# Performance work log

Measured on AMD Instinct MI355X. Metric: run time of the kernel, lower is better.

Reference implementation:

```python
import jax, jax.numpy as jnp
import numpy as np

K = 8  # repeat(1,1,1,9) in the source forces k+1 == 9
LRELU_SLOPE = 0.01  # nn.LeakyReLU default negative slope


def knn_idx(x, k):
    """x: [B, C, N] -> indices of k nearest points [B, N, k] (largest neg sq dist)."""
    xx = jnp.sum(x * x, axis=1)                       # [B, N]
    inner = jnp.einsum('bcn,bcm->bnm', x, x)          # [B, N, N]
    neg_sq_dist = 2.0 * inner - xx[:, :, None] - xx[:, None, :]
    return jax.lax.top_k(neg_sq_dist, k)[1]           # [B, N, k]


def gather_neighbors(feat, idx):
    """feat: [B, C, N], idx: [B, N, k] -> [B, C, N, k] (grouping_operation)."""
    return jax.vmap(lambda f, i: f[:, i])(feat, idx)


def setup_inputs() -> dict:
    key = jax.random.key(0)
    k1, k2, k3 = jax.random.split(key, 3)
    B, C, N = 8, 128, 4096
    points = jax.random.normal(k1, (B, C, N), dtype=jnp.float32)
    # xavier_uniform-ish init for W [C, 1]
    limit = 1.414 * np.sqrt(6.0 / (C + 1))
    W = jax.random.uniform(k2, (C, 1), dtype=jnp.float32, minval=-limit, maxval=limit)
    conv2_w = jax.random.normal(k3, (C, C), dtype=jnp.float32) * 0.05
    return {"points": points, "W": W, "conv2_w": conv2_w}


def reference(points, W, conv2_w):
    # points: [B, C, N]
    shortcut = points
    # knn on raw (detached) features -> integer indices, no grad path
    idx = knn_idx(jax.lax.stop_gradient(points), K)            # [B, N, K]
    features = jax.nn.leaky_relu(points, LRELU_SLOPE)          # [B, C, N]
    grouped_points = gather_neighbors(features, idx)           # [B, C, N, K]
    center_points = features[:, :, :, None]                    # [B, C, N, 1]
    feats = jnp.concatenate([grouped_points, center_points], axis=3)  # [B, C, N, K+1]
    feats = jnp.transpose(feats, (0, 2, 3, 1))                 # [B, N, K+1, C]
    att = jnp.einsum('bnkc,co->bnko', feats, W)                # [B, N, K+1, 1]
    att = jax.nn.softmax(att, axis=2)                          # softmax over K+1 neighbors
    # repeat(1,1,1,9) then matmul: out[b,n,i,c] = att[b,n,i] * sum_j feats[b,n,j,c]
    # followed by mean over i -> mean_i(att) * sum_j(feats)
    s = jnp.sum(feats, axis=2)                                 # [B, N, C]
    out = jnp.mean(att, axis=2) * s                            # [B, N, C]
    out = jnp.transpose(out, (0, 2, 1)) + shortcut             # [B, C, N]
    # 1x1 conv residual branch on grouped neighbor features
    grouped_points_nn = jnp.einsum('oc,bcnk->bonk', conv2_w, grouped_points)  # [B, C, N, K]
    return (out, grouped_points_nn)
```

## Files before the change

### kernel.cpp

```cpp
#include <hip/hip_runtime.h>
#include <cstdint>
#include <cstddef>

#define BB_ 8
#define CC_ 128
#define NN_ 4096
#define KK_ 8

#define XX_OFF  0
#define IDX_OFF 32768
#define G_OFF   294912

__device__ __forceinline__ float lrelu(float v) { return v >= 0.f ? v : 0.01f * v; }

template <int S>
__device__ __forceinline__ void insert_tieup(float (&v)[S], int (&ix)[S], float d, int m) {
  if (d < v[S - 1]) return;
  bool bs[S];
#pragma unroll
  for (int s = 0; s < S; ++s) bs[s] = (v[s] > d);
#pragma unroll
  for (int s = S - 1; s >= 1; --s) {
    v[s]  = bs[s] ? v[s]  : (bs[s - 1] ? d : v[s - 1]);
    ix[s] = bs[s] ? ix[s] : (bs[s - 1] ? m : ix[s - 1]);
  }
  if (!bs[0]) { v[0] = d; ix[0] = m; }
}

template <int S>
__device__ __forceinline__ void insert_ti_desc(float (&v)[S], int (&ix)[S], float d, int m) {
  bool stay = (v[S - 1] > d) || (v[S - 1] == d && ix[S - 1] > m);
  if (stay) return;
  bool bs[S];
#pragma unroll
  for (int s = 0; s < S; ++s) bs[s] = (v[s] > d) || (v[s] == d && ix[s] > m);
#pragma unroll
  for (int s = S - 1; s >= 1; --s) {
    v[s]  = bs[s] ? v[s]  : (bs[s - 1] ? d : v[s - 1]);
    ix[s] = bs[s] ? ix[s] : (bs[s - 1] ? m : ix[s - 1]);
  }
  if (!bs[0]) { v[0] = d; ix[0] = m; }
}

__global__ void k_xx(const float* __restrict__ x, float* __restrict__ out1f) {
  int t = blockIdx.x * 256 + threadIdx.x;
  int b = t >> 12, n = t & (NN_ - 1);
  const float* p = x + ((size_t)b * CC_) * NN_ + n;
  float acc = 0.f;
  {
#pragma clang fp contract(off)
#pragma unroll
    for (int c = 0; c < CC_; ++c) {
      float v = p[(size_t)c * NN_];
      float v2 = v * v;
      acc = acc + v2;
    }
  }
  out1f[XX_OFF + t] = acc;
}

__global__ __launch_bounds__(256, 2) void k_knn(const float* __restrict__ x,
                                                float* __restrict__ out1f) {
  __shared__ __align__(16) union S {
    struct {
      float As[64][132];
      float Bs[64][132];
      float xxm[64];
    } a;
    struct { float v[64 * 129]; int i[64 * 129]; } mg;
  } s;

  const float* xxz = out1f + XX_OFF;
  int* idxz = (int*)(out1f + IDX_OFF);

  const int blk = blockIdx.x;
  const int b = blk >> 6;
  const int n0 = (blk & 63) << 6;
  const float* xb = x + ((size_t)b * CC_) * NN_;
  const int t = threadIdx.x;
  const int tr = t & 15, tc = t >> 4;

  {
    int r = t & 63, c0 = t >> 6;
    for (int c = c0; c < CC_; c += 4) s.a.As[r][c] = xb[(size_t)c * NN_ + n0 + r];
  }

  float xr[4];
#pragma unroll
  for (int i = 0; i < 4; ++i) xr[i] = xxz[(b << 12) + n0 + tr + 16 * i];

  float lv[4][8]; int li[4][8];
#pragma unroll
  for (int i = 0; i < 4; ++i)
#pragma unroll
    for (int q = 0; q < 8; ++q) { lv[i][q] = -INFINITY; li[i][q] = 0x7FFFFFFF; }

  for (int m0 = 0; m0 < NN_; m0 += 64) {
    __syncthreads();
    {
      int ml = t & 63, c1 = t >> 6;
      for (int c = c1; c < CC_; c += 4) s.a.Bs[ml][c] = xb[(size_t)c * NN_ + m0 + ml];
      if (t < 64) s.a.xxm[t] = xxz[(b << 12) + m0 + t];
    }
    __syncthreads();

    float acc[4][4] = {};
#pragma unroll 2
    for (int cq = 0; cq < CC_; cq += 4) {
      float4 av[4], bv[4];
#pragma unroll
      for (int i = 0; i < 4; ++i)
        av[i] = *reinterpret_cast<const float4*>(&s.a.As[tr + 16 * i][cq]);
#pragma unroll
      for (int j = 0; j < 4; ++j)
        bv[j] = *reinterpret_cast<const float4*>(&s.a.Bs[tc * 4 + j][cq]);
#pragma unroll
      for (int i = 0; i < 4; ++i)
#pragma unroll
        for (int j = 0; j < 4; ++j) {
          acc[i][j] = fmaf(av[i].x, bv[j].x, acc[i][j]);
          acc[i][j] = fmaf(av[i].y, bv[j].y, acc[i][j]);
          acc[i][j] = fmaf(av[i].z, bv[j].z, acc[i][j]);
          acc[i][j] = fmaf(av[i].w, bv[j].w, acc[i][j]);
        }
    }

#pragma unroll
    for (int j = 0; j < 4; ++j) {
      float xm = s.a.xxm[tc * 4 + j];
      int m = m0 + tc * 4 + j;
#pragma unroll
      for (int i = 0; i < 4; ++i) {
        float d = (2.0f * acc[i][j] - xr[i]) - xm;
        insert_tieup<8>(lv[i], li[i], d, m);
      }
    }
  }

  __syncthreads();
#pragma unroll
  for (int i = 0; i < 4; ++i) {
    int base = (tr + 16 * i) * 129 + (tc << 3);
#pragma unroll
    for (int q = 0; q < 8; ++q) {
      s.mg.v[base + q] = lv[i][q];
      s.mg.i[base + q] = li[i][q];
    }
  }
  __syncthreads();
  if (t < 64) {
    float bv[8]; int bi[8];
#pragma unroll
    for (int q = 0; q < 8; ++q) { bv[q] = -INFINITY; bi[q] = 0x7FFFFFFF; }
    const float* cv = s.mg.v + t * 129;
    const int*   ci = s.mg.i + t * 129;
    for (int q = 0; q < 128; ++q) {
      insert_ti_desc<8>(bv, bi, cv[q], ci[q]);
    }
    int* op = idxz + (b << 15) + ((n0 + t) << 3);
#pragma unroll
    for (int q = 0; q < KK_; ++q) op[q] = bi[q];
  }
}

__global__ __launch_bounds__(256) void k_gemm(const float* __restrict__ x,
                                              const float* __restrict__ w2,
                                              float* __restrict__ out1f) {
  __shared__ __align__(16) float Ws[64][68];
  __shared__ __align__(16) float Fs[64][68];
  int bb = blockIdx.x >> 7;
  int r = blockIdx.x & 127;
  int o0 = (r >> 6) << 6;
  int m0 = (r & 63) << 6;
  const float* xb = x + ((size_t)bb * CC_) * NN_;
  float* gb = out1f + G_OFF + ((size_t)bb * CC_) * NN_;
  int t = threadIdx.x;
  int tm = t & 15, to = t >> 4;

  float acc[4][4] = {};
  for (int cc = 0; cc < CC_; cc += 64) {
    __syncthreads();
    {
      int cl = t & 63, q0 = t >> 6;
      for (int oo = q0; oo < 64; oo += 4) Ws[oo][cl] = w2[(o0 + oo) * CC_ + cc + cl];
      for (int c2 = q0; c2 < 64; c2 += 4) Fs[cl][c2] = lrelu(xb[(size_t)(cc + c2) * NN_ + m0 + cl]);
    }
    __syncthreads();
#pragma unroll 8
    for (int cq = 0; cq < 64; cq += 4) {
      float4 aw[4], bf[4];
#pragma unroll
      for (int i = 0; i < 4; ++i) aw[i] = *reinterpret_cast<const float4*>(&Ws[to + 16 * i][cq]);
#pragma unroll
      for (int j = 0; j < 4; ++j) bf[j] = *reinterpret_cast<const float4*>(&Fs[tm + 16 * j][cq]);
#pragma unroll
      for (int i = 0; i < 4; ++i)
#pragma unroll
        for (int j = 0; j < 4; ++j) {
          acc[i][j] = fmaf(aw[i].x, bf[j].x, acc[i][j]);
          acc[i][j] = fmaf(aw[i].y, bf[j].y, acc[i][j]);
          acc[i][j] = fmaf(aw[i].z, bf[j].z, acc[i][j]);
          acc[i][j] = fmaf(aw[i].w, bf[j].w, acc[i][j]);
        }
    }
  }
#pragma unroll
  for (int i = 0; i < 4; ++i)
#pragma unroll
    for (int j = 0; j < 4; ++j)
      gb[((size_t)(o0 + to + 16 * i)) * NN_ + m0 + tm + 16 * j] = acc[i][j];
}

__global__ void k_out0(const float* __restrict__ x, const float* __restrict__ out1f,
                       float* __restrict__ out) {
  __shared__ int idxL[512];
  int b = blockIdx.x >> 6, nt = blockIdx.x & 63;
  int n0 = nt << 6;
  int t = threadIdx.x;
  const int* ib = (const int*)(out1f + IDX_OFF) + (b << 15) + (n0 << 3);
  idxL[t] = ib[t];
  idxL[t + 256] = ib[t + 256];
  __syncthreads();
  int nl = t & 63, c0 = t >> 6;
  for (int c = c0; c < CC_; c += 4) {
    const float* row = x + ((size_t)b * CC_ + c) * NN_;
    float self = row[n0 + nl];
    float s = 0.f;
#pragma unroll
    for (int k = 0; k < KK_; ++k) s += lrelu(row[idxL[(nl << 3) + k]]);
    s += lrelu(self);
    out[((size_t)b * CC_ + c) * NN_ + n0 + nl] = fmaf(s, 1.0f / 9.0f, self);
  }
}

__global__ void k_gatherA(float* __restrict__ out1f) {
  int bc = 137 + blockIdx.x;
  int b = bc >> 7;
  const int* idxz = (const int*)(out1f + IDX_OFF) + (b << 15);
  const float* gs = out1f + G_OFF + (size_t)bc * (size_t)NN_;
  float* op = out1f + (size_t)bc * 32768;
  for (int e = threadIdx.x; e < 32768; e += 256) {
    op[e] = gs[idxz[e]];
  }
}

__global__ __launch_bounds__(256) void k_gatherB(const float* __restrict__ x,
                                                 const float* __restrict__ w2,
                                                 float* __restrict__ out1f) {
  __shared__ int idxL[512];
  __shared__ float xcols[8][128];
  int T = blockIdx.x;
  int t = threadIdx.x;
  const int* idxz = (const int*)(out1f + IDX_OFF);
  idxL[t]       = idxz[0 * 32768 + ((T * 32) << 3) + t];
  idxL[t + 256] = idxz[1 * 32768 + ((T * 32) << 3) + t];
  __syncthreads();

  for (int it = 0; it < 64; ++it) {
    int colbase = it * 8;
    {
      int cg = t >> 5, lane = t & 31;
      int col = colbase + cg;
      int bsel = col >> 8;
      int m = idxL[col];
      const float* xb = x + ((size_t)bsel * CC_) * NN_;
#pragma unroll
      for (int q = 0; q < 4; ++q) {
        int c = lane + 32 * q;
        xcols[cg][c] = lrelu(xb[(size_t)c * NN_ + m]);
      }
    }
    __syncthreads();
    {
      int cg = t >> 5, c0 = t & 31;
      int col = colbase + cg;
      int bsel = col >> 8;
      int rk = col & 255;
      int n = T * 32 + (rk >> 3);
      int k = rk & 7;
      int hmax = (bsel == 0) ? 4 : 1;
      for (int h = 0; h < hmax; ++h) {
        int c = c0 + 32 * h;
        const float* wr = w2 + c * CC_;
        float acc = 0.f;
#pragma unroll 8
        for (int cc = 0; cc < CC_; ++cc) acc = fmaf(wr[cc], xcols[cg][cc], acc);
        if (bsel == 0 || c <= 8) {
          out1f[(size_t)(bsel * CC_ + c) * 32768 + (n << 3) + k] = acc;
        }
      }
    }
    __syncthreads();
  }
}

extern "C" void kernel_launch(void* const* d_in, const int* in_sizes, int n_in,
                              void* d_out, int out_size, void* d_ws, size_t ws_size,
                              hipStream_t stream) {
  const float* x  = (const float*)d_in[0];
  const float* w2 = (const float*)d_in[2];

  float* out0  = (float*)d_out;
  float* out1f = out0 + (size_t)BB_ * CC_ * NN_;
  (void)d_ws; (void)ws_size;

  k_xx     <<<(BB_ * NN_) / 256,  256, 0, stream>>>(x, out1f);
  k_knn    <<<BB_ * (NN_ / 64),   256, 0, stream>>>(x, out1f);
  k_gemm   <<<BB_ * 128,          256, 0, stream>>>(x, w2, out1f);
  k_out0   <<<BB_ * 64,           256, 0, stream>>>(x, out1f, out0);
  k_gatherA<<<1024 - 137,         256, 0, stream>>>(out1f);
  k_gatherB<<<128,                256, 0, stream>>>(x, w2, out1f);
}
```

Before: 2.182 ms.

## Swizzle KNN shared-memory tiles and double-buffer LDS reads in the dot loop

Replaces the padded [64][132] shared tiles with unpadded 128-wide rows whose float4 groups are XOR-swizzled by row, so the strided LDS float4 reads avoid bank conflicts. The inner product loop is rewritten to register double-buffer the next float4 group while computing FMAs on the current one. This is meant to cut LDS bank-conflict stalls and hide LDS latency in the distance GEMM. In exchange it needs more live registers under launch_bounds(256,2), and the index arithmetic gets more complex.

```diff
diff --git a/kernel.cpp b/kernel.cpp
--- a/kernel.cpp
+++ b/kernel.cpp
@@ -59,12 +59,39 @@
   out1f[XX_OFF + t] = acc;
 }
 
+__device__ __forceinline__ int swzw(int r, int c) {
+  return (r << 7) + ((((c >> 2) ^ (r & 15)) << 2) | (c & 3));
+}
+
+__device__ __forceinline__ void fma16(float (&acc)[4][4], const float4 (&a)[4],
+                                      const float4 (&b)[4]) {
+#pragma unroll
+  for (int i = 0; i < 4; ++i)
+#pragma unroll
+    for (int j = 0; j < 4; ++j) {
+      acc[i][j] = fmaf(a[i].x, b[j].x, acc[i][j]);
+      acc[i][j] = fmaf(a[i].y, b[j].y, acc[i][j]);
+      acc[i][j] = fmaf(a[i].z, b[j].z, acc[i][j]);
+      acc[i][j] = fmaf(a[i].w, b[j].w, acc[i][j]);
+    }
+}
+
+__device__ __forceinline__ void load8(float4 (&a)[4], float4 (&b)[4],
+                                      const float4* AsV, const float4* BsV,
+                                      const int (&baseA)[4], const int (&baseB)[4],
+                                      const int (&keyB)[4], int tr, int g) {
+#pragma unroll
+  for (int i = 0; i < 4; ++i) a[i] = AsV[baseA[i] + (g ^ tr)];
+#pragma unroll
+  for (int j = 0; j < 4; ++j) b[j] = BsV[baseB[j] + (g ^ keyB[j])];
+}
+
 __global__ __launch_bounds__(256, 2) void k_knn(const float* __restrict__ x,
                                                 float* __restrict__ out1f) {
   __shared__ __align__(16) union S {
     struct {
-      float As[64][132];
-      float Bs[64][132];
+      float As[64 * 128];
+      float Bs[64 * 128];
       float xxm[64];
     } a;
     struct { float v[64 * 129]; int i[64 * 129]; } mg;
@@ -82,7 +109,7 @@
 
   {
     int r = t & 63, c0 = t >> 6;
-    for (int c = c0; c < CC_; c += 4) s.a.As[r][c] = xb[(size_t)c * NN_ + n0 + r];
+    for (int c = c0; c < CC_; c += 4) s.a.As[swzw(r, c)] = xb[(size_t)c * NN_ + n0 + r];
   }
 
   float xr[4];
@@ -94,36 +121,40 @@
   for (int i = 0; i < 4; ++i)
 #pragma unroll
     for (int q = 0; q < 8; ++q) { lv[i][q] = -INFINITY; li[i][q] = 0x7FFFFFFF; }
+
+  const float4* AsV = reinterpret_cast<const float4*>(s.a.As);
+  const float4* BsV = reinterpret_cast<const float4*>(s.a.Bs);
+  int baseA[4], baseB[4], keyB[4];
+#pragma unroll
+  for (int i = 0; i < 4; ++i) baseA[i] = (tr + 16 * i) * 32;
+#pragma unroll
+  for (int j = 0; j < 4; ++j) {
+    int rB = tc * 4 + j;
+    baseB[j] = rB * 32;
+    keyB[j] = rB & 15;
+  }
 
   for (int m0 = 0; m0 < NN_; m0 += 64) {
     __syncthreads();
     {
       int ml = t & 63, c1 = t >> 6;
-      for (int c = c1; c < CC_; c += 4) s.a.Bs[ml][c] = xb[(size_t)c * NN_ + m0 + ml];
+      for (int c = c1; c < CC_; c += 4) s.a.Bs[swzw(ml, c)] = xb[(size_t)c * NN_ + m0 + ml];
       if (t < 64) s.a.xxm[t] = xxz[(b << 12) + m0 + t];
     }
     __syncthreads();
 
     float acc[4][4] = {};
-#pragma unroll 2
-    for (int cq = 0; cq < CC_; cq += 4) {
-      float4 av[4], bv[4];
-#pragma unroll
-      for (int i = 0; i < 4; ++i)
-        av[i] = *reinterpret_cast<const float4*>(&s.a.As[tr + 16 * i][cq]);
-#pragma unroll
-      for (int j = 0; j < 4; ++j)
-        bv[j] = *reinterpret_cast<const float4*>(&s.a.Bs[tc * 4 + j][cq]);
-#pragma unroll
-      for (int i = 0; i < 4; ++i)
-#pragma unroll
-        for (int j = 0; j < 4; ++j) {
-          acc[i][j] = fmaf(av[i].x, bv[j].x, acc[i][j]);
-          acc[i][j] = fmaf(av[i].y, bv[j].y, acc[i][j]);
-          acc[i][j] = fmaf(av[i].z, bv[j].z, acc[i][j]);
-          acc[i][j] = fmaf(av[i].w, bv[j].w, acc[i][j]);
-        }
-    }
+    float4 a0[4], b0[4], a1[4], b1[4];
+    load8(a0, b0, AsV, BsV, baseA, baseB, keyB, tr, 0);
+    for (int g = 0; g < 30; g += 2) {
+      load8(a1, b1, AsV, BsV, baseA, baseB, keyB, tr, g + 1);
+      fma16(acc, a0, b0);
+      load8(a0, b0, AsV, BsV, baseA, baseB, keyB, tr, g + 2);
+      fma16(acc, a1, b1);
+    }
+    load8(a1, b1, AsV, BsV, baseA, baseB, keyB, tr, 31);
+    fma16(acc, a0, b0);
+    fma16(acc, a1, b1);
 
 #pragma unroll
     for (int j = 0; j < 4; ++j) {
```

After: 2.288 ms. +4.9%, slower.

## Shrink kNN shared memory, split B tile in halves, merge top-k via shuffles

Applied to the files above, without the earlier changes.

The kNN kernel now stages the B tile in two 64-channel halves, which cuts its shared-memory footprint so three blocks can fit per CU (launch bounds raised to 3). Global-to-shared loads are packed into float4 stores. The final top-k merge uses wave shuffles and a small per-wave shared buffer instead of one thread scanning 128 candidates. The cost is an extra pair of barriers per m-tile and tighter register pressure under the higher occupancy target.

```diff
diff --git a/kernel.cpp b/kernel.cpp
--- a/kernel.cpp
+++ b/kernel.cpp
@@ -59,15 +59,28 @@
   out1f[XX_OFF + t] = acc;
 }
 
-__global__ __launch_bounds__(256, 2) void k_knn(const float* __restrict__ x,
+__device__ __forceinline__ void fma16(float (&acc)[4][4], const float4 (&a)[4],
+                                      const float4 (&b)[4]) {
+#pragma unroll
+  for (int i = 0; i < 4; ++i)
+#pragma unroll
+    for (int j = 0; j < 4; ++j) {
+      acc[i][j] = fmaf(a[i].x, b[j].x, acc[i][j]);
+      acc[i][j] = fmaf(a[i].y, b[j].y, acc[i][j]);
+      acc[i][j] = fmaf(a[i].z, b[j].z, acc[i][j]);
+      acc[i][j] = fmaf(a[i].w, b[j].w, acc[i][j]);
+    }
+}
+
+__global__ __launch_bounds__(256, 3) void k_knn(const float* __restrict__ x,
                                                 float* __restrict__ out1f) {
   __shared__ __align__(16) union S {
     struct {
-      float As[64][132];
-      float Bs[64][132];
+      float As[64 * 132];
+      float Bs[64 * 68];
       float xxm[64];
     } a;
-    struct { float v[64 * 129]; int i[64 * 129]; } mg;
+    struct { float v[4 * 64 * 9]; int i[4 * 64 * 9]; } mg;
   } s;
 
   const float* xxz = out1f + XX_OFF;
@@ -79,10 +92,19 @@
   const float* xb = x + ((size_t)b * CC_) * NN_;
   const int t = threadIdx.x;
   const int tr = t & 15, tc = t >> 4;
+  const int r64 = t & 63, wv = t >> 6;
 
   {
-    int r = t & 63, c0 = t >> 6;
-    for (int c = c0; c < CC_; c += 4) s.a.As[r][c] = xb[(size_t)c * NN_ + n0 + r];
+#pragma unroll
+    for (int q = 0; q < 8; ++q) {
+      int g = wv + 4 * q;
+      float4 tmp;
+      tmp.x = xb[(size_t)(4 * g + 0) * NN_ + n0 + r64];
+      tmp.y = xb[(size_t)(4 * g + 1) * NN_ + n0 + r64];
+      tmp.z = xb[(size_t)(4 * g + 2) * NN_ + n0 + r64];
+      tmp.w = xb[(size_t)(4 * g + 3) * NN_ + n0 + r64];
+      *reinterpret_cast<float4*>(&s.a.As[r64 * 132 + 4 * g]) = tmp;
+    }
   }
 
   float xr[4];
@@ -95,34 +117,44 @@
 #pragma unroll
     for (int q = 0; q < 8; ++q) { lv[i][q] = -INFINITY; li[i][q] = 0x7FFFFFFF; }
 
+  const float4* As4 = reinterpret_cast<const float4*>(s.a.As);
+  const float4* Bs4 = reinterpret_cast<const float4*>(s.a.Bs);
+  int rowA[4], rowB[4];
+#pragma unroll
+  for (int i = 0; i < 4; ++i) rowA[i] = (tr + 16 * i) * 33;
+#pragma unroll
+  for (int j = 0; j < 4; ++j) rowB[j] = (tc * 4 + j) * 17;
+
   for (int m0 = 0; m0 < NN_; m0 += 64) {
-    __syncthreads();
-    {
-      int ml = t & 63, c1 = t >> 6;
-      for (int c = c1; c < CC_; c += 4) s.a.Bs[ml][c] = xb[(size_t)c * NN_ + m0 + ml];
-      if (t < 64) s.a.xxm[t] = xxz[(b << 12) + m0 + t];
-    }
-    __syncthreads();
-
     float acc[4][4] = {};
+#pragma unroll
+    for (int p = 0; p < 2; ++p) {
+      __syncthreads();
+      {
+#pragma unroll
+        for (int q = 0; q < 4; ++q) {
+          int gl = wv + 4 * q;
+          int c0 = 64 * p + 4 * gl;
+          float4 tmp;
+          tmp.x = xb[(size_t)(c0 + 0) * NN_ + m0 + r64];
+          tmp.y = xb[(size_t)(c0 + 1) * NN_ + m0 + r64];
+          tmp.z = xb[(size_t)(c0 + 2) * NN_ + m0 + r64];
+          tmp.w = xb[(size_t)(c0 + 3) * NN_ + m0 + r64];
+          *reinterpret_cast<float4*>(&s.a.Bs[r64 * 68 + 4 * gl]) = tmp;
+        }
+        if (p == 0 && t < 64) s.a.xxm[t] = xxz[(b << 12) + m0 + t];
+      }
+      __syncthreads();
+
 #pragma unroll 2
-    for (int cq = 0; cq < CC_; cq += 4) {
-      float4 av[4], bv[4];
-#pragma unroll
-      for (int i = 0; i < 4; ++i)
-        av[i] = *reinterpret_cast<const float4*>(&s.a.As[tr + 16 * i][cq]);
-#pragma unroll
-      for (int j = 0; j < 4; ++j)
-        bv[j] = *reinterpret_cast<const float4*>(&s.a.Bs[tc * 4 + j][cq]);
-#pragma unroll
-      for (int i = 0; i < 4; ++i)
-#pragma unroll
-        for (int j = 0; j < 4; ++j) {
-          acc[i][j] = fmaf(av[i].x, bv[j].x, acc[i][j]);
-          acc[i][j] = fmaf(av[i].y, bv[j].y, acc[i][j]);
-          acc[i][j] = fmaf(av[i].z, bv[j].z, acc[i][j]);
-          acc[i][j] = fmaf(av[i].w, bv[j].w, acc[i][j]);
-        }
+      for (int gl = 0; gl < 16; ++gl) {
+        float4 av[4], bv[4];
+#pragma unroll
+        for (int i = 0; i < 4; ++i) av[i] = As4[rowA[i] + 16 * p + gl];
+#pragma unroll
+        for (int j = 0; j < 4; ++j) bv[j] = Bs4[rowB[j] + gl];
+        fma16(acc, av, bv);
+      }
     }
 
 #pragma unroll
@@ -139,27 +171,44 @@
 
   __syncthreads();
 #pragma unroll
-  for (int i = 0; i < 4; ++i) {
-    int base = (tr + 16 * i) * 129 + (tc << 3);
-#pragma unroll
-    for (int q = 0; q < 8; ++q) {
-      s.mg.v[base + q] = lv[i][q];
-      s.mg.i[base + q] = li[i][q];
+  for (int mk = 16; mk <= 32; mk <<= 1) {
+#pragma unroll
+    for (int i = 0; i < 4; ++i) {
+      float pv[8]; int pi[8];
+#pragma unroll
+      for (int q = 0; q < 8; ++q) {
+        pv[q] = __shfl_xor(lv[i][q], mk, 64);
+        pi[q] = __shfl_xor(li[i][q], mk, 64);
+      }
+#pragma unroll
+      for (int q = 0; q < 8; ++q) insert_ti_desc<8>(lv[i], li[i], pv[q], pi[q]);
+    }
+  }
+  if ((t & 63) < 16) {
+#pragma unroll
+    for (int i = 0; i < 4; ++i) {
+      int base = wv * 576 + (tr + 16 * i) * 9;
+#pragma unroll
+      for (int q = 0; q < 8; ++q) {
+        s.mg.v[base + q] = lv[i][q];
+        s.mg.i[base + q] = li[i][q];
+      }
     }
   }
   __syncthreads();
   if (t < 64) {
-    float bv[8]; int bi[8];
-#pragma unroll
-    for (int q = 0; q < 8; ++q) { bv[q] = -INFINITY; bi[q] = 0x7FFFFFFF; }
-    const float* cv = s.mg.v + t * 129;
-    const int*   ci = s.mg.i + t * 129;
-    for (int q = 0; q < 128; ++q) {
-      insert_ti_desc<8>(bv, bi, cv[q], ci[q]);
+    float bvv[8]; int bii[8];
+#pragma unroll
+    for (int q = 0; q < 8; ++q) { bvv[q] = s.mg.v[t * 9 + q]; bii[q] = s.mg.i[t * 9 + q]; }
+#pragma unroll
+    for (int w = 1; w < 4; ++w) {
+      int base = w * 576 + t * 9;
+#pragma unroll
+      for (int q = 0; q < 8; ++q) insert_ti_desc<8>(bvv, bii, s.mg.v[base + q], s.mg.i[base + q]);
     }
     int* op = idxz + (b << 15) + ((n0 + t) << 3);
 #pragma unroll
-    for (int q = 0; q < KK_; ++q) op[q] = bi[q];
+    for (int q = 0; q < KK_; ++q) op[q] = bii[q];
   }
 }
 
```

Result: slower. 2.522 ms (+15.6%).
